# Performance work log

Measured on AMD Instinct MI355X. Metric: run time of the kernel, lower is better.

## Reference

```python
import jax, jax.numpy as jnp
import numpy as np

MODEL_DIM = 2048
NUM_HEADS = 32
NUM_KV_HEADS = 8
HEAD_DIM = MODEL_DIM // NUM_HEADS  # 64
NUM_REP = NUM_HEADS // NUM_KV_HEADS  # 4


def setup_inputs() -> dict:
    key = jax.random.key(0)
    ks = jax.random.split(key, 6)
    B, S = 1, 2048
    s = 1.0 / np.sqrt(MODEL_DIM)
    x = jax.random.normal(ks[0], (B, S, MODEL_DIM), dtype=jnp.float32)
    # causal mask, 1 = keep, 0 = mask (scores.masked_fill(mask == 0, -1e9))
    mask = jnp.tril(jnp.ones((S, S), dtype=jnp.int32))[None, None, :, :]
    w_q = jax.random.normal(ks[1], (MODEL_DIM, MODEL_DIM), dtype=jnp.float32) * s
    w_k = jax.random.normal(ks[2], (NUM_KV_HEADS * HEAD_DIM, MODEL_DIM), dtype=jnp.float32) * s
    w_v = jax.random.normal(ks[3], (NUM_KV_HEADS * HEAD_DIM, MODEL_DIM), dtype=jnp.float32) * s
    w_o = jax.random.normal(ks[4], (MODEL_DIM, MODEL_DIM), dtype=jnp.float32) * s
    b_o = jax.random.normal(ks[5], (MODEL_DIM,), dtype=jnp.float32) * 0.01
    return {"x": x, "mask": mask, "w_q": w_q, "w_k": w_k, "w_v": w_v, "w_o": w_o, "b_o": b_o}


def reference(x, mask, w_q, w_k, w_v, w_o, b_o):
    B, S, _ = x.shape
    # projections (torch Linear: x @ W.T)
    q = (x @ w_q.T).reshape(B, S, NUM_HEADS, HEAD_DIM).transpose(0, 2, 1, 3)      # [B,H,S,D]
    k = (x @ w_k.T).reshape(B, S, NUM_KV_HEADS, HEAD_DIM).transpose(0, 2, 1, 3)   # [B,Hk,S,D]
    v = (x @ w_v.T).reshape(B, S, NUM_KV_HEADS, HEAD_DIM).transpose(0, 2, 1, 3)   # [B,Hk,S,D]
    # group Q heads by their shared KV head instead of materializing repeated KV
    qg = q.reshape(B, NUM_KV_HEADS, NUM_REP, S, HEAD_DIM)                         # [B,Hk,R,S,D]
    scale = 1.0 / np.sqrt(HEAD_DIM).astype(np.float32)
    scores = jnp.einsum('bgrsd,bgtd->bgrst', qg, k) * scale                       # [B,Hk,R,S,S]
    scores = jnp.where(mask[:, :, None, :, :] == 0, jnp.float32(-1e9), scores)
    attn = jax.nn.softmax(scores, axis=-1)
    ctx = jnp.einsum('bgrst,bgtd->bgrsd', attn, v)                                # [B,Hk,R,S,D]
    ctx = ctx.reshape(B, NUM_HEADS, S, HEAD_DIM).transpose(0, 2, 1, 3).reshape(B, S, MODEL_DIM)
    return ctx @ w_o.T + b_o
```

## Files before the change

kernel.cpp:

```cpp
#include <hip/hip_runtime.h>
#include <hip/hip_bf16.h>

typedef __hip_bfloat16 bf16;
typedef __attribute__((ext_vector_type(8))) short short8;
typedef __attribute__((ext_vector_type(4))) short short4_t;
typedef __attribute__((ext_vector_type(4))) float f32x4;

#define S_LEN 2048
#define DMODEL 2048
#define NH 32
#define NKV 8
#define DH 64

__global__ void detect_kernel(const unsigned int* __restrict__ x, int* __restrict__ flag) {
    int tid = threadIdx.x;
    unsigned int w = x[tid * 37];
    int e0 = (w >> 7) & 0xFF;
    int in = (e0 >= 100 && e0 <= 140) ? 1 : 0;
    unsigned long long m = __ballot(in);
    if (tid == 0) flag[0] = (__popcll(m) >= 48) ? 1 : 0;
}

__device__ __forceinline__ void conv8(const void* src, bf16* dst, int i, float scale, int isbf) {
    short8 out;
    if (isbf) {
        short8 v = *(const short8*)((const bf16*)src + i);
        if (scale != 1.0f) {
            #pragma unroll
            for (int j = 0; j < 8; ++j) {
                float f = __bfloat162float(((const bf16*)&v)[j]) * scale;
                ((bf16*)&out)[j] = __float2bfloat16(f);
            }
        } else out = v;
    } else {
        const float* gp = (const float*)src + i;
        f32x4 a = *(const f32x4*)gp;
        f32x4 b = *(const f32x4*)(gp + 4);
        #pragma unroll
        for (int j = 0; j < 4; ++j) ((bf16*)&out)[j]     = __float2bfloat16(a[j] * scale);
        #pragma unroll
        for (int j = 0; j < 4; ++j) ((bf16*)&out)[j + 4] = __float2bfloat16(b[j] * scale);
    }
    *(short8*)(dst + i) = out;
}

__global__ __launch_bounds__(256)
void convert_kernel(const void* __restrict__ src, bf16* __restrict__ dst,
                    int n, float scale, const int* __restrict__ flagp) {
    const int isbf = flagp[0];
    int i = (blockIdx.x * 256 + threadIdx.x) * 8;
    const int stride = gridDim.x * 256 * 8;
    for (; i < n; i += stride) conv8(src, dst, i, scale, isbf);
}

__global__ __launch_bounds__(256)
void convert4_kernel(const void* __restrict__ x, const void* __restrict__ wq,
                     const void* __restrict__ wk, const void* __restrict__ wv,
                     bf16* __restrict__ xb, bf16* __restrict__ wqkv,
                     const int* __restrict__ flagp) {
    const int isbf = flagp[0];
    const int b = blockIdx.x;
    const void* src; bf16* dst; int boff; float scale = 1.0f;
    if (b < 2048)       { src = x;  dst = xb;              boff = b;        }
    else if (b < 4096)  { src = wq; dst = wqkv;            boff = b - 2048; scale = 0.125f; }
    else if (b < 4608)  { src = wk; dst = wqkv + 4194304;  boff = b - 4096; }
    else                { src = wv; dst = wqkv + 5242880;  boff = b - 4608; }
    int i = (boff * 256 + threadIdx.x) * 8;
    conv8(src, dst, i, scale, isbf);
}

__device__ __forceinline__ void gload_lds16(const void* g, void* l) {
    __builtin_amdgcn_global_load_lds(
        (const __attribute__((address_space(1))) void*)(unsigned long long)(size_t)g,
        (__attribute__((address_space(3))) void*)(unsigned int)(size_t)l,
        16, 0, 0);
}

__device__ __forceinline__ void gemm_core_2ph(const bf16* __restrict__ A, const bf16* __restrict__ B,
                                              int K, int m0, int n0,
                                              bf16* sA, bf16* sB, f32x4 acc[4][2]) {
    const int tid = threadIdx.x;
    const int w = tid >> 6, lane = tid & 63;
    const int wm = (w >> 1) * 64, wn = (w & 1) * 32;
    const int lm = lane & 15, lq = lane >> 4;
    const int xr = lm & 7;

    size_t aoff[4], boff[2];
    #pragma unroll
    for (int r = 0; r < 4; ++r) {
        int ci = w * 256 + r * 64 + lane;
        int row = ci >> 3, c = (ci & 7) ^ (row & 7);
        aoff[r] = (size_t)(m0 + row) * K + c * 8;
    }
    #pragma unroll
    for (int r = 0; r < 2; ++r) {
        int cj = w * 128 + r * 64 + lane;
        int row = cj >> 3, c = (cj & 7) ^ (row & 7);
        boff[r] = (size_t)(n0 + row) * K + c * 8;
    }

    const int nt = K >> 6;
    int cur = 0;

    {
        bf16* la = sA + w * 2048;
        bf16* lb = sB + w * 1024;
        #pragma unroll
        for (int r = 0; r < 4; ++r) gload_lds16(A + aoff[r], la + r * 512);
        #pragma unroll
        for (int r = 0; r < 2; ++r) gload_lds16(B + boff[r], lb + r * 512);
    }
    __syncthreads();

    for (int t = 0; t < nt; ++t) {
        bf16* curA = sA + cur * 8192;
        bf16* curB = sB + cur * 4096;
        if (t + 1 < nt) {
            const int nxt = cur ^ 1;
            const int k0 = (t + 1) << 6;
            bf16* la = sA + nxt * 8192 + w * 2048;
            bf16* lb = sB + nxt * 4096 + w * 1024;
            #pragma unroll
            for (int r = 0; r < 4; ++r) gload_lds16(A + aoff[r] + k0, la + r * 512);
            #pragma unroll
            for (int r = 0; r < 2; ++r) gload_lds16(B + boff[r] + k0, lb + r * 512);
        }

        short8 aF[2][4], bF[2][2];
        #pragma unroll
        for (int ks = 0; ks < 2; ++ks) {
            const int cc = ((ks * 4 + lq) ^ xr) * 8;
            #pragma unroll
            for (int i = 0; i < 4; ++i)
                aF[ks][i] = *(const short8*)&curA[(wm + i * 16 + lm) * 64 + cc];
            #pragma unroll
            for (int j = 0; j < 2; ++j)
                bF[ks][j] = *(const short8*)&curB[(wn + j * 16 + lm) * 64 + cc];
        }

        __builtin_amdgcn_s_setprio(1);
        #pragma unroll
        for (int ks = 0; ks < 2; ++ks)
            #pragma unroll
            for (int i = 0; i < 4; ++i)
                #pragma unroll
                for (int j = 0; j < 2; ++j)
                    acc[i][j] = __builtin_amdgcn_mfma_f32_16x16x32_bf16(aF[ks][i], bF[ks][j], acc[i][j], 0, 0, 0);
        __builtin_amdgcn_s_setprio(0);

        __syncthreads();
        cur ^= 1;
    }
}

template<bool BIAS, bool BIAS_DYN, bool OUT_DYN>
__global__ __launch_bounds__(256, 3)
void gemm_bf16s(const bf16* __restrict__ A, const bf16* __restrict__ B,
                const void* __restrict__ bias, void* __restrict__ C,
                int M, int N, int K, int ldc, const int* __restrict__ flagp) {
    __shared__ bf16 sA[2 * 128 * 64];
    __shared__ bf16 sB[2 * 64 * 64];
    const int isbf = flagp[0];
    const int tid = threadIdx.x;
    const int m0 = blockIdx.y * 128, n0 = blockIdx.x * 64;
    const int w = tid >> 6, lane = tid & 63;
    const int wm = (w >> 1) * 64, wn = (w & 1) * 32;
    const int lm = lane & 15, lq = lane >> 4;

    f32x4 acc[4][2];
    const f32x4 zero = {0.f, 0.f, 0.f, 0.f};
    for (int i = 0; i < 4; ++i)
        for (int j = 0; j < 2; ++j) acc[i][j] = zero;

    gemm_core_2ph(A, B, K, m0, n0, sA, sB, acc);

    for (int i = 0; i < 4; ++i)
        for (int j = 0; j < 2; ++j)
            for (int r = 0; r < 4; ++r) {
                int row = m0 + wm + i * 16 + lq * 4 + r;
                int col = n0 + wn + j * 16 + lm;
                float v = acc[i][j][r];
                if (BIAS) {
                    if (BIAS_DYN && !isbf) v += ((const float*)bias)[col];
                    else                   v += __bfloat162float(((const bf16*)bias)[col]);
                }
                size_t idx = (size_t)row * ldc + col;
                if (OUT_DYN && !isbf) ((float*)C)[idx] = v;
                else                  ((bf16*)C)[idx] = __float2bfloat16(v);
            }
}

__global__ __launch_bounds__(256, 3)
void gemm_qkv(const bf16* __restrict__ A, const bf16* __restrict__ B,
              bf16* __restrict__ Qo, bf16* __restrict__ Ko, bf16* __restrict__ Vto) {
    __shared__ bf16 sA[2 * 128 * 64];
    __shared__ bf16 sB[2 * 64 * 64];
    const int tid = threadIdx.x;
    const int m0 = blockIdx.y * 128, n0 = blockIdx.x * 64;
    const int w = tid >> 6, lane = tid & 63;
    const int wm = (w >> 1) * 64, wn = (w & 1) * 32;
    const int lm = lane & 15, lq = lane >> 4;

    f32x4 acc[4][2];
    const f32x4 zero = {0.f, 0.f, 0.f, 0.f};
    for (int i = 0; i < 4; ++i)
        for (int j = 0; j < 2; ++j) acc[i][j] = zero;

    gemm_core_2ph(A, B, DMODEL, m0, n0, sA, sB, acc);

    const int route = (n0 < 2048) ? 0 : ((n0 < 2560) ? 1 : 2);
    for (int i = 0; i < 4; ++i)
        for (int j = 0; j < 2; ++j)
            for (int r = 0; r < 4; ++r) {
                int row = m0 + wm + i * 16 + lq * 4 + r;
                int col = n0 + wn + j * 16 + lm;
                bf16 v = __float2bfloat16(acc[i][j][r]);
                if (route == 0)      Qo[(size_t)row * DMODEL + col] = v;
                else if (route == 1) Ko[(size_t)row * (NKV * DH) + (col - 2048)] = v;
                else                 Vto[(size_t)(col - 2560) * S_LEN + row] = v;
            }
}

template<bool TRANS_OUT, bool BIAS, bool A_DYN, bool B_DYN, bool BIAS_DYN, bool OUT_DYN>
__global__ __launch_bounds__(256, 2)
void gemm_bt(const void* __restrict__ A, const void* __restrict__ B,
             const void* __restrict__ bias, void* __restrict__ C,
             int M, int N, int K, int ldc, const int* __restrict__ flagp) {
    __shared__ bf16 sA[128 * 32];
    __shared__ bf16 sB[128 * 32];

    const int isbf = flagp[0];
    const int tid = threadIdx.x;
    const int m0 = blockIdx.y * 128, n0 = blockIdx.x * 128;
    const int w = tid >> 6, lane = tid & 63;
    const int wm = (w >> 1) * 64, wn = (w & 1) * 64;
    const int lm = lane & 15, lq = lane >> 4;

    f32x4 acc[4][4];
    const f32x4 zero = {0.f, 0.f, 0.f, 0.f};
    for (int i = 0; i < 4; ++i)
        for (int j = 0; j < 4; ++j) acc[i][j] = zero;

    for (int k0 = 0; k0 < K; k0 += 32) {
        __syncthreads();
        for (int it = 0; it < 2; ++it) {
            int c = it * 256 + tid;
            int row = c >> 2, off = (c & 3) * 8;
            if (!A_DYN || isbf) {
                *(short8*)&sA[row * 32 + off] =
                    *(const short8*)((const bf16*)A + (size_t)(m0 + row) * K + k0 + off);
            } else {
                const float* gp = (const float*)A + (size_t)(m0 + row) * K + k0 + off;
                #pragma unroll
                for (int i = 0; i < 8; ++i) sA[row * 32 + off + i] = __float2bfloat16(gp[i]);
            }
            if (!B_DYN || isbf) {
                *(short8*)&sB[row * 32 + off] =
                    *(const short8*)((const bf16*)B + (size_t)(n0 + row) * K + k0 + off);
            } else {
                const float* gp = (const float*)B + (size_t)(n0 + row) * K + k0 + off;
                #pragma unroll
                for (int i = 0; i < 8; ++i) sB[row * 32 + off + i] = __float2bfloat16(gp[i]);
            }
        }
        __syncthreads();

        short8 aF[4], bF[4];
        for (int i = 0; i < 4; ++i)
            aF[i] = *(const short8*)&sA[(wm + i * 16 + lm) * 32 + lq * 8];
        for (int i = 0; i < 4; ++i)
            bF[i] = *(const short8*)&sB[(wn + i * 16 + lm) * 32 + lq * 8];
        for (int i = 0; i < 4; ++i)
            for (int j = 0; j < 4; ++j)
                acc[i][j] = __builtin_amdgcn_mfma_f32_16x16x32_bf16(aF[i], bF[j], acc[i][j], 0, 0, 0);
    }

    for (int i = 0; i < 4; ++i)
        for (int j = 0; j < 4; ++j)
            for (int r = 0; r < 4; ++r) {
                int row = m0 + wm + i * 16 + lq * 4 + r;
                int col = n0 + wn + j * 16 + lm;
                float v = acc[i][j][r];
                if (BIAS) {
                    if (BIAS_DYN && !isbf) v += ((const float*)bias)[col];
                    else                   v += __bfloat162float(((const bf16*)bias)[col]);
                }
                size_t idx = TRANS_OUT ? (size_t)col * ldc + row : (size_t)row * ldc + col;
                if (OUT_DYN && !isbf) ((float*)C)[idx] = v;
                else                  ((bf16*)C)[idx] = __float2bfloat16(v);
            }
}

template<bool PRESCALED>
__global__ __launch_bounds__(256, 2)
void attn_kernel(const bf16* __restrict__ Q, const bf16* __restrict__ Km,
                 const bf16* __restrict__ Vt, bf16* __restrict__ ctx) {
    __shared__ bf16 sQ[64 * 72];
    __shared__ bf16 sK[64 * 72];
    __shared__ bf16 sV[64 * 72];
    __shared__ bf16 sP[4][16 * 72];

    const int tid = threadIdx.x;
    const int h  = blockIdx.y;
    const int kvh = h >> 2;
    const int w = tid >> 6, lane = tid & 63;
    const int lm = lane & 15, lq = lane >> 4;
    const int qloc = w * 16 + lm;

    const int r0 = tid >> 3,         o0 = (tid & 7) * 8;
    const int r1 = (tid + 256) >> 3, o1 = (tid & 7) * 8;

    const f32x4 zero = {0.f, 0.f, 0.f, 0.f};

    for (int ph = 0; ph < 2; ++ph) {
        const int qb = ph ? (31 - blockIdx.x) : blockIdx.x;

        __syncthreads();
        for (int c = tid; c < 512; c += 256) {
            int row = c >> 3, off = (c & 7) * 8;
            *(short8*)&sQ[row * 72 + off] =
                *(const short8*)&Q[(size_t)(qb * 64 + row) * DMODEL + h * 64 + off];
        }

        float m_r = -1e30f, l_r = 0.f;
        f32x4 oacc[4];
        #pragma unroll
        for (int ni = 0; ni < 4; ++ni) oacc[ni] = zero;

        short8 kr0, kr1, vr0, vr1;
        kr0 = *(const short8*)&Km[(size_t)r0 * (NKV * DH) + kvh * 64 + o0];
        kr1 = *(const short8*)&Km[(size_t)r1 * (NKV * DH) + kvh * 64 + o1];
        vr0 = *(const short8*)&Vt[(size_t)(kvh * 64 + r0) * S_LEN + o0];
        vr1 = *(const short8*)&Vt[(size_t)(kvh * 64 + r1) * S_LEN + o1];

        for (int kt = 0; kt <= qb; ++kt) {
            __syncthreads();
            *(short8*)&sK[r0 * 72 + o0] = kr0;
            *(short8*)&sK[r1 * 72 + o1] = kr1;
            *(short8*)&sV[r0 * 72 + o0] = vr0;
            *(short8*)&sV[r1 * 72 + o1] = vr1;
            __syncthreads();
            if (kt < qb) {
                int nk = kt + 1;
                kr0 = *(const short8*)&Km[(size_t)(nk * 64 + r0) * (NKV * DH) + kvh * 64 + o0];
                kr1 = *(const short8*)&Km[(size_t)(nk * 64 + r1) * (NKV * DH) + kvh * 64 + o1];
                vr0 = *(const short8*)&Vt[(size_t)(kvh * 64 + r0) * S_LEN + nk * 64 + o0];
                vr1 = *(const short8*)&Vt[(size_t)(kvh * 64 + r1) * S_LEN + nk * 64 + o1];
            }

            f32x4 sacc[4];
            #pragma unroll
            for (int ni = 0; ni < 4; ++ni) sacc[ni] = zero;
            __builtin_amdgcn_s_setprio(1);
            #pragma unroll
            for (int ks = 0; ks < 2; ++ks) {
                short8 aq = *(const short8*)&sQ[(w * 16 + lm) * 72 + ks * 32 + lq * 8];
                #pragma unroll
                for (int ni = 0; ni < 4; ++ni) {
                    short8 bk = *(const short8*)&sK[(ni * 16 + lm) * 72 + ks * 32 + lq * 8];
                    sacc[ni] = __builtin_amdgcn_mfma_f32_16x16x32_bf16(bk, aq, sacc[ni], 0, 0, 0);
                }
            }
            __builtin_amdgcn_s_setprio(0);

            float sv[4][4];
            float mx = -3e38f;
            #pragma unroll
            for (int ni = 0; ni < 4; ++ni)
                #pragma unroll
                for (int r = 0; r < 4; ++r) {
                    float s = sacc[ni][r];
                    if (!PRESCALED) s *= 0.125f;
                    if (kt == qb && (ni * 16 + lq * 4 + r) > qloc) s = -1e30f;
                    sv[ni][r] = s;
                    mx = fmaxf(mx, s);
                }
            mx = fmaxf(mx, __shfl_xor(mx, 16));
            mx = fmaxf(mx, __shfl_xor(mx, 32));

            int defer = (mx - m_r <= 8.0f) ? 1 : 0;
            if (!__all(defer)) {
                float m_new = fmaxf(m_r, mx);
                float alpha = __expf(m_r - m_new);
                m_r = m_new;
                l_r *= alpha;
                #pragma unroll
                for (int r = 0; r < 4; ++r) {
                    float a_b = __shfl(alpha, (lane & 48) | (lq * 4 + r));
                    #pragma unroll
                    for (int ni = 0; ni < 4; ++ni) oacc[ni][r] *= a_b;
                }
            }

            float rs = 0.f;
            #pragma unroll
            for (int ni = 0; ni < 4; ++ni) {
                short4_t pk;
                #pragma unroll
                for (int r = 0; r < 4; ++r) {
                    float p = __expf(sv[ni][r] - m_r);
                    rs += p;
                    ((bf16*)&pk)[r] = __float2bfloat16(p);
                }
                *(short4_t*)&sP[w][lm * 72 + ni * 16 + lq * 4] = pk;
            }
            rs += __shfl_xor(rs, 16);
            rs += __shfl_xor(rs, 32);
            l_r += rs;

            asm volatile("s_waitcnt lgkmcnt(0)" ::: "memory");
            __builtin_amdgcn_sched_barrier(0);

            __builtin_amdgcn_s_setprio(1);
            #pragma unroll
            for (int ks = 0; ks < 2; ++ks) {
                short8 ap = *(const short8*)&sP[w][lm * 72 + ks * 32 + lq * 8];
                #pragma unroll
                for (int ni = 0; ni < 4; ++ni) {
                    short8 bv = *(const short8*)&sV[(ni * 16 + lm) * 72 + ks * 32 + lq * 8];
                    oacc[ni] = __builtin_amdgcn_mfma_f32_16x16x32_bf16(ap, bv, oacc[ni], 0, 0, 0);
                }
            }
            __builtin_amdgcn_s_setprio(0);
        }

        #pragma unroll
        for (int r = 0; r < 4; ++r) {
            float l_b = __shfl(l_r, (lane & 48) | (lq * 4 + r));
            float inv = 1.0f / l_b;
            #pragma unroll
            for (int ni = 0; ni < 4; ++ni)
                ctx[(size_t)(qb * 64 + w * 16 + lq * 4 + r) * DMODEL + h * 64 + ni * 16 + lm] =
                    __float2bfloat16(oacc[ni][r] * inv);
        }
    }
}

extern "C" void kernel_launch(void* const* d_in, const int* in_sizes, int n_in,
                              void* d_out, int out_size, void* d_ws, size_t ws_size,
                              hipStream_t stream) {
    const void* x   = d_in[0];
    const void* w_q = d_in[2];
    const void* w_k = d_in[3];
    const void* w_v = d_in[4];
    const void* w_o = d_in[5];
    const void* b_o = d_in[6];

    const size_t MB = 1024u * 1024u;
    char* ws = (char*)d_ws;
    int*  flag = (int*)ws;
    dim3 blk(256);

    detect_kernel<<<1, 64, 0, stream>>>((const unsigned int*)x, flag);

    if (ws_size >= 32 * MB + 4096) {
        bf16* xb   = (bf16*)(ws + 4096);
        bf16* wqkv = (bf16*)(ws + 4096 + 8 * MB);
        bf16* Qws  = (bf16*)(ws + 4096 + 20 * MB);
        bf16* Kws  = (bf16*)(ws + 4096 + 28 * MB);
        bf16* Vtws = (bf16*)(ws + 4096 + 30 * MB);
        bf16* wob  = xb;
        bf16* Ctx  = wqkv;

        convert4_kernel<<<5120, blk, 0, stream>>>(x, w_q, w_k, w_v, xb, wqkv, flag);
        gemm_qkv<<<dim3(48, 16), blk, 0, stream>>>(xb, wqkv, Qws, Kws, Vtws);
        convert_kernel<<<2048, blk, 0, stream>>>(w_o, wob, DMODEL * DMODEL, 1.0f, flag);
        attn_kernel<true><<<dim3(16, 32), blk, 0, stream>>>(Qws, Kws, Vtws, Ctx);
        gemm_bf16s<true, true, true><<<dim3(32, 16), blk, 0, stream>>>(
            Ctx, wob, b_o, d_out, S_LEN, DMODEL, DMODEL, DMODEL, flag);
    } else {
        bf16* Qws  = (bf16*)(ws + 4096);
        bf16* Kws  = (bf16*)(ws + 4096 + 8u * MB);
        bf16* Vtws = (bf16*)(ws + 4096 + 10u * MB);
        bf16* Ctx  = (bf16*)(ws + 4096 + 12u * MB);

        gemm_bt<false, false, true, true, false, false><<<dim3(16, 16), blk, 0, stream>>>(
            x, w_q, nullptr, Qws, S_LEN, DMODEL, DMODEL, DMODEL, flag);
        gemm_bt<false, false, true, true, false, false><<<dim3(4, 16), blk, 0, stream>>>(
            x, w_k, nullptr, Kws, S_LEN, NKV * DH, DMODEL, NKV * DH, flag);
        gemm_bt<true, false, true, true, false, false><<<dim3(4, 16), blk, 0, stream>>>(
            x, w_v, nullptr, Vtws, S_LEN, NKV * DH, DMODEL, S_LEN, flag);
        attn_kernel<false><<<dim3(16, 32), blk, 0, stream>>>(Qws, Kws, Vtws, Ctx);
        gemm_bt<false, true, false, true, true, true><<<dim3(16, 16), blk, 0, stream>>>(
            Ctx, w_o, b_o, d_out, S_LEN, DMODEL, DMODEL, DMODEL, flag);
    }
}
```

Measured before the change: 225.0 us.

## Split attention KV loop across two wave groups with split-K softmax merge

The attention block grows to 512 threads, made of two groups of four waves. Each group handles alternating KV tiles of the same query tile, keeping its own K/V shared buffers and online-softmax state. At the end the partial outputs and (max, sum) pairs are merged through shared memory before the context is written. This doubles the waves working on each query tile to shorten the serial KV loop and raise occupancy, at the cost of more LDS, an extra merge step with syncs, and idle waves on odd tile counts.

After: 221.8 us. No clear change (-1.4%).

```diff
diff --git a/kernel.cpp b/kernel.cpp
--- a/kernel.cpp
+++ b/kernel.cpp
@@ -292,32 +292,42 @@
 }
 
 template<bool PRESCALED>
-__global__ __launch_bounds__(256, 2)
+__global__ __launch_bounds__(512, 4)
 void attn_kernel(const bf16* __restrict__ Q, const bf16* __restrict__ Km,
                  const bf16* __restrict__ Vt, bf16* __restrict__ ctx) {
     __shared__ bf16 sQ[64 * 72];
-    __shared__ bf16 sK[64 * 72];
-    __shared__ bf16 sV[64 * 72];
-    __shared__ bf16 sP[4][16 * 72];
+    __shared__ bf16 sK[2][64 * 72];
+    __shared__ bf16 sV[2][64 * 72];
+    __shared__ bf16 sP[8][16 * 72];
 
     const int tid = threadIdx.x;
     const int h  = blockIdx.y;
     const int kvh = h >> 2;
-    const int w = tid >> 6, lane = tid & 63;
+    const int w = tid >> 6;
+    const int g = w >> 2;
+    const int wv = w & 3;
+    const int lane = tid & 63;
     const int lm = lane & 15, lq = lane >> 4;
-    const int qloc = w * 16 + lm;
-
-    const int r0 = tid >> 3,         o0 = (tid & 7) * 8;
-    const int r1 = (tid + 256) >> 3, o1 = (tid & 7) * 8;
+    const int qloc = wv * 16 + lm;
+
+    const int tg = tid & 255;
+    const int r0 = tg >> 3,         o0 = (tg & 7) * 8;
+    const int r1 = (tg + 256) >> 3, o1 = (tg & 7) * 8;
+
+    float* xO  = (float*)&sK[0][0];
+    float* xs0 = (float*)&sV[0][0];
+    float* xs1 = xs0 + 128;
 
     const f32x4 zero = {0.f, 0.f, 0.f, 0.f};
 
     for (int ph = 0; ph < 2; ++ph) {
         const int qb = ph ? (31 - blockIdx.x) : blockIdx.x;
+        const int nt = qb + 1;
+        const int niter = (nt + 1) >> 1;
 
         __syncthreads();
-        for (int c = tid; c < 512; c += 256) {
-            int row = c >> 3, off = (c & 7) * 8;
+        {
+            int row = tid >> 3, off = (tid & 7) * 8;
             *(short8*)&sQ[row * 72 + off] =
                 *(const short8*)&Q[(size_t)(qb * 64 + row) * DMODEL + h * 64 + off];
         }
@@ -328,110 +338,156 @@
         for (int ni = 0; ni < 4; ++ni) oacc[ni] = zero;
 
         short8 kr0, kr1, vr0, vr1;
-        kr0 = *(const short8*)&Km[(size_t)r0 * (NKV * DH) + kvh * 64 + o0];
-        kr1 = *(const short8*)&Km[(size_t)r1 * (NKV * DH) + kvh * 64 + o1];
-        vr0 = *(const short8*)&Vt[(size_t)(kvh * 64 + r0) * S_LEN + o0];
-        vr1 = *(const short8*)&Vt[(size_t)(kvh * 64 + r1) * S_LEN + o1];
-
-        for (int kt = 0; kt <= qb; ++kt) {
+        {
+            const int b0 = g * 64;
+            kr0 = *(const short8*)&Km[(size_t)(b0 + r0) * (NKV * DH) + kvh * 64 + o0];
+            kr1 = *(const short8*)&Km[(size_t)(b0 + r1) * (NKV * DH) + kvh * 64 + o1];
+            vr0 = *(const short8*)&Vt[(size_t)(kvh * 64 + r0) * S_LEN + b0 + o0];
+            vr1 = *(const short8*)&Vt[(size_t)(kvh * 64 + r1) * S_LEN + b0 + o1];
+        }
+
+        for (int i = 0; i < niter; ++i) {
+            const int kt = 2 * i + g;
+            const bool act = kt < nt;
+
             __syncthreads();
-            *(short8*)&sK[r0 * 72 + o0] = kr0;
-            *(short8*)&sK[r1 * 72 + o1] = kr1;
-            *(short8*)&sV[r0 * 72 + o0] = vr0;
-            *(short8*)&sV[r1 * 72 + o1] = vr1;
+            *(short8*)&sK[g][r0 * 72 + o0] = kr0;
+            *(short8*)&sK[g][r1 * 72 + o1] = kr1;
+            *(short8*)&sV[g][r0 * 72 + o0] = vr0;
+            *(short8*)&sV[g][r1 * 72 + o1] = vr1;
             __syncthreads();
-            if (kt < qb) {
-                int nk = kt + 1;
-                kr0 = *(const short8*)&Km[(size_t)(nk * 64 + r0) * (NKV * DH) + kvh * 64 + o0];
-                kr1 = *(const short8*)&Km[(size_t)(nk * 64 + r1) * (NKV * DH) + kvh * 64 + o1];
-                vr0 = *(const short8*)&Vt[(size_t)(kvh * 64 + r0) * S_LEN + nk * 64 + o0];
-                vr1 = *(const short8*)&Vt[(size_t)(kvh * 64 + r1) * S_LEN + nk * 64 + o1];
-            }
-
-            f32x4 sacc[4];
-            #pragma unroll
-            for (int ni = 0; ni < 4; ++ni) sacc[ni] = zero;
-            __builtin_amdgcn_s_setprio(1);
-            #pragma unroll
-            for (int ks = 0; ks < 2; ++ks) {
-                short8 aq = *(const short8*)&sQ[(w * 16 + lm) * 72 + ks * 32 + lq * 8];
+
+            if (i + 1 < niter) {
+                int b0 = (kt + 2) * 64;
+                b0 = b0 > (S_LEN - 64) ? (S_LEN - 64) : b0;
+                kr0 = *(const short8*)&Km[(size_t)(b0 + r0) * (NKV * DH) + kvh * 64 + o0];
+                kr1 = *(const short8*)&Km[(size_t)(b0 + r1) * (NKV * DH) + kvh * 64 + o1];
+                vr0 = *(const short8*)&Vt[(size_t)(kvh * 64 + r0) * S_LEN + b0 + o0];
+                vr1 = *(const short8*)&Vt[(size_t)(kvh * 64 + r1) * S_LEN + b0 + o1];
+            }
+
+            if (act) {
+                f32x4 sacc[4];
+                #pragma unroll
+                for (int ni = 0; ni < 4; ++ni) sacc[ni] = zero;
+                __builtin_amdgcn_s_setprio(1);
+                #pragma unroll
+                for (int ks = 0; ks < 2; ++ks) {
+                    short8 aq = *(const short8*)&sQ[(wv * 16 + lm) * 72 + ks * 32 + lq * 8];
+                    #pragma unroll
+                    for (int ni = 0; ni < 4; ++ni) {
+                        short8 bk = *(const short8*)&sK[g][(ni * 16 + lm) * 72 + ks * 32 + lq * 8];
+                        sacc[ni] = __builtin_amdgcn_mfma_f32_16x16x32_bf16(bk, aq, sacc[ni], 0, 0, 0);
+                    }
+                }
+                __builtin_amdgcn_s_setprio(0);
+
+                float mx = -3e38f;
+                if (kt == nt - 1) {
+                    const int qrel = qloc;
+                    #pragma unroll
+                    for (int ni = 0; ni < 4; ++ni)
+                        #pragma unroll
+                        for (int r = 0; r < 4; ++r) {
+                            float s = sacc[ni][r];
+                            if (!PRESCALED) s *= 0.125f;
+                            if ((ni * 16 + lq * 4 + r) > qrel) s = -1e30f;
+                            sacc[ni][r] = s;
+                            mx = fmaxf(mx, s);
+                        }
+                } else {
+                    #pragma unroll
+                    for (int ni = 0; ni < 4; ++ni)
+                        #pragma unroll
+                        for (int r = 0; r < 4; ++r) {
+                            float s = sacc[ni][r];
+                            if (!PRESCALED) s *= 0.125f;
+                            sacc[ni][r] = s;
+                            mx = fmaxf(mx, s);
+                        }
+                }
+                mx = fmaxf(mx, __shfl_xor(mx, 16));
+                mx = fmaxf(mx, __shfl_xor(mx, 32));
+
+                int defer = (mx - m_r <= 8.0f) ? 1 : 0;
+                if (!__all(defer)) {
+                    float m_new = fmaxf(m_r, mx);
+                    float alpha = __expf(m_r - m_new);
+                    m_r = m_new;
+                    l_r *= alpha;
+                    #pragma unroll
+                    for (int r = 0; r < 4; ++r) {
+                        float a_b = __shfl(alpha, (lane & 48) | (lq * 4 + r));
+                        #pragma unroll
+                        for (int ni = 0; ni < 4; ++ni) oacc[ni][r] *= a_b;
+                    }
+                }
+
+                float rs = 0.f;
                 #pragma unroll
                 for (int ni = 0; ni < 4; ++ni) {
-                    short8 bk = *(const short8*)&sK[(ni * 16 + lm) * 72 + ks * 32 + lq * 8];
-                    sacc[ni] = __builtin_amdgcn_mfma_f32_16x16x32_bf16(bk, aq, sacc[ni], 0, 0, 0);
-                }
-            }
-            __builtin_amdgcn_s_setprio(0);
-
-            float sv[4][4];
-            float mx = -3e38f;
+                    short4_t pk;
+                    #pragma unroll
+                    for (int r = 0; r < 4; ++r) {
+                        float p = __expf(sacc[ni][r] - m_r);
+                        rs += p;
+                        ((bf16*)&pk)[r] = __float2bfloat16(p);
+                    }
+                    *(short4_t*)&sP[w][lm * 72 + ni * 16 + lq * 4] = pk;
+                }
+                rs += __shfl_xor(rs, 16);
+                rs += __shfl_xor(rs, 32);
+                l_r += rs;
+
+                asm volatile("s_waitcnt lgkmcnt(0)" ::: "memory");
+                __builtin_amdgcn_sched_barrier(0);
+
+                __builtin_amdgcn_s_setprio(1);
+                #pragma unroll
+                for (int ks = 0; ks < 2; ++ks) {
+                    short8 ap = *(const short8*)&sP[w][lm * 72 + ks * 32 + lq * 8];
+                    #pragma unroll
+                    for (int ni = 0; ni < 4; ++ni) {
+                        short8 bv = *(const short8*)&sV[g][(ni * 16 + lm) * 72 + ks * 32 + lq * 8];
+                        oacc[ni] = __builtin_amdgcn_mfma_f32_16x16x32_bf16(ap, bv, oacc[ni], 0, 0, 0);
+                    }
+                }
+                __builtin_amdgcn_s_setprio(0);
+            }
+        }
+
+        __syncthreads();
+        if (g == 1) {
             #pragma unroll
             for (int ni = 0; ni < 4; ++ni)
                 #pragma unroll
-                for (int r = 0; r < 4; ++r) {
-                    float s = sacc[ni][r];
-                    if (!PRESCALED) s *= 0.125f;
-                    if (kt == qb && (ni * 16 + lq * 4 + r) > qloc) s = -1e30f;
-                    sv[ni][r] = s;
-                    mx = fmaxf(mx, s);
-                }
-            mx = fmaxf(mx, __shfl_xor(mx, 16));
-            mx = fmaxf(mx, __shfl_xor(mx, 32));
-
-            int defer = (mx - m_r <= 8.0f) ? 1 : 0;
-            if (!__all(defer)) {
-                float m_new = fmaxf(m_r, mx);
-                float alpha = __expf(m_r - m_new);
-                m_r = m_new;
-                l_r *= alpha;
-                #pragma unroll
-                for (int r = 0; r < 4; ++r) {
-                    float a_b = __shfl(alpha, (lane & 48) | (lq * 4 + r));
-                    #pragma unroll
-                    for (int ni = 0; ni < 4; ++ni) oacc[ni][r] *= a_b;
-                }
-            }
-
-            float rs = 0.f;
-            #pragma unroll
-            for (int ni = 0; ni < 4; ++ni) {
-                short4_t pk;
-                #pragma unroll
-                for (int r = 0; r < 4; ++r) {
-                    float p = __expf(sv[ni][r] - m_r);
-                    rs += p;
-                    ((bf16*)&pk)[r] = __float2bfloat16(p);
-                }
-                *(short4_t*)&sP[w][lm * 72 + ni * 16 + lq * 4] = pk;
-            }
-            rs += __shfl_xor(rs, 16);
-            rs += __shfl_xor(rs, 32);
-            l_r += rs;
-
-            asm volatile("s_waitcnt lgkmcnt(0)" ::: "memory");
-            __builtin_amdgcn_sched_barrier(0);
-
-            __builtin_amdgcn_s_setprio(1);
-            #pragma unroll
-            for (int ks = 0; ks < 2; ++ks) {
-                short8 ap = *(const short8*)&sP[w][lm * 72 + ks * 32 + lq * 8];
+                for (int r = 0; r < 4; ++r)
+                    xO[(wv * 64 + lane) * 16 + ni * 4 + r] = oacc[ni][r];
+            if (lq == 0) {
+                xs1[(wv * 16 + lm) * 2]     = m_r;
+                xs1[(wv * 16 + lm) * 2 + 1] = l_r;
+            }
+        } else if (lq == 0) {
+            xs0[(wv * 16 + lm) * 2]     = m_r;
+            xs0[(wv * 16 + lm) * 2 + 1] = l_r;
+        }
+        __syncthreads();
+        if (g == 0) {
+            #pragma unroll
+            for (int r = 0; r < 4; ++r) {
+                const int row = wv * 16 + lq * 4 + r;
+                float m0 = xs0[row * 2], l0 = xs0[row * 2 + 1];
+                float m1 = xs1[row * 2], l1 = xs1[row * 2 + 1];
+                float mm = fmaxf(m0, m1);
+                float w0 = __expf(m0 - mm), w1 = __expf(m1 - mm);
+                float inv = 1.0f / (w0 * l0 + w1 * l1);
                 #pragma unroll
                 for (int ni = 0; ni < 4; ++ni) {
-                    short8 bv = *(const short8*)&sV[(ni * 16 + lm) * 72 + ks * 32 + lq * 8];
-                    oacc[ni] = __builtin_amdgcn_mfma_f32_16x16x32_bf16(ap, bv, oacc[ni], 0, 0, 0);
-                }
-            }
-            __builtin_amdgcn_s_setprio(0);
-        }
-
-        #pragma unroll
-        for (int r = 0; r < 4; ++r) {
-            float l_b = __shfl(l_r, (lane & 48) | (lq * 4 + r));
-            float inv = 1.0f / l_b;
-            #pragma unroll
-            for (int ni = 0; ni < 4; ++ni)
-                ctx[(size_t)(qb * 64 + w * 16 + lq * 4 + r) * DMODEL + h * 64 + ni * 16 + lm] =
-                    __float2bfloat16(oacc[ni][r] * inv);
+                    float o1 = xO[(wv * 64 + lane) * 16 + ni * 4 + r];
+                    ctx[(size_t)(qb * 64 + row) * DMODEL + h * 64 + ni * 16 + lm] =
+                        __float2bfloat16((w0 * oacc[ni][r] + w1 * o1) * inv);
+                }
+            }
         }
     }
 }
@@ -465,7 +521,7 @@
         convert4_kernel<<<5120, blk, 0, stream>>>(x, w_q, w_k, w_v, xb, wqkv, flag);
         gemm_qkv<<<dim3(48, 16), blk, 0, stream>>>(xb, wqkv, Qws, Kws, Vtws);
         convert_kernel<<<2048, blk, 0, stream>>>(w_o, wob, DMODEL * DMODEL, 1.0f, flag);
-        attn_kernel<true><<<dim3(16, 32), blk, 0, stream>>>(Qws, Kws, Vtws, Ctx);
+        attn_kernel<true><<<dim3(16, 32), dim3(512), 0, stream>>>(Qws, Kws, Vtws, Ctx);
         gemm_bf16s<true, true, true><<<dim3(32, 16), blk, 0, stream>>>(
             Ctx, wob, b_o, d_out, S_LEN, DMODEL, DMODEL, DMODEL, flag);
     } else {
@@ -480,7 +536,7 @@
             x, w_k, nullptr, Kws, S_LEN, NKV * DH, DMODEL, NKV * DH, flag);
         gemm_bt<true, false, true, true, false, false><<<dim3(4, 16), blk, 0, stream>>>(
             x, w_v, nullptr, Vtws, S_LEN, NKV * DH, DMODEL, S_LEN, flag);
-        attn_kernel<false><<<dim3(16, 32), blk, 0, stream>>>(Qws, Kws, Vtws, Ctx);
+        attn_kernel<false><<<dim3(16, 32), dim3(512), 0, stream>>>(Qws, Kws, Vtws, Ctx);
         gemm_bt<false, true, false, true, true, true><<<dim3(16, 16), blk, 0, stream>>>(
             Ctx, w_o, b_o, d_out, S_LEN, DMODEL, DMODEL, DMODEL, flag);
     }
```
